# Kernel optimization log

Measured on AMD Instinct MI355X. Metric: run time of the kernel, lower is better.

## Reference

```python
import jax, jax.numpy as jnp
import numpy as np
import math


def proxy_delta_linear(x, W, gain):
    # x: [B,T,Din], W: [Dout,Din], gain: [1,1,Dout]
    D = x.shape[-1]
    xa = jnp.tanh(x)
    wa = jnp.tanh(W)
    x_sq = jnp.sum(xa * xa, axis=-1, keepdims=True)          # [B,T,1]
    w_sq = jnp.sum(wa * wa, axis=-1)                          # [Dout]
    dot = jnp.einsum('btd,od->bto', xa, wa)                   # [B,T,Dout]
    l2_sq = jnp.clip(x_sq + w_sq - 2.0 * dot, 0.0)
    out = 1.0 - l2_sq / D
    return (out - 0.5) * gain


def setup_inputs() -> dict:
    key = jax.random.key(0)
    ks = jax.random.split(key, 6)
    B, T, C = 2, 2048, 1024
    return {
        'x':  jax.random.normal(ks[0], (B, T, C), dtype=jnp.float32),
        'Wq': jax.random.normal(ks[1], (C, C), dtype=jnp.float32) * 0.02,
        'gq': jnp.full((1, 1, C), 2.0, dtype=jnp.float32),
        'Wk': jax.random.normal(ks[2], (C, C), dtype=jnp.float32) * 0.02,
        'gk': jnp.full((1, 1, C), 2.0, dtype=jnp.float32),
        'Wv': jax.random.normal(ks[3], (C, C), dtype=jnp.float32) * 0.02,
        'gv': jnp.full((1, 1, C), 2.0, dtype=jnp.float32),
        'Wo': jax.random.normal(ks[4], (C, C), dtype=jnp.float32) * 0.02,
    }


def reference(x, Wq, gq, Wk, gk, Wv, gv, Wo):
    B, T, C = x.shape
    H = 16
    D = C // H
    scale = math.sqrt(D)
    q = jnp.tanh(proxy_delta_linear(x, Wq, gq)).reshape(B, T, H, D).transpose(0, 2, 1, 3)
    k = jnp.tanh(proxy_delta_linear(x, Wk, gk)).reshape(B, T, H, D).transpose(0, 2, 1, 3)
    v = proxy_delta_linear(x, Wv, gv).reshape(B, T, H, D).transpose(0, 2, 1, 3)
    q_sq = jnp.sum(q * q, axis=-1, keepdims=True)             # [B,H,T,1]
    k_sq = jnp.sum(k * k, axis=-1)[:, :, None, :]             # [B,H,1,T]
    dot = jnp.einsum('bhtd,bhsd->bhts', q, k)                 # [B,H,T,T]
    dist_sq = jnp.clip(q_sq + k_sq - 2.0 * dot, 0.0)
    logits = -dist_sq / (scale * 10.0)
    attn = jax.nn.softmax(logits, axis=-1)
    out = jnp.einsum('bhts,bhsd->bhtd', attn, v)
    out = out.transpose(0, 2, 1, 3).reshape(B, T, C)
    return jnp.einsum('btc,oc->bto', out, Wo)
```

## Files before the change

kernel.cpp:

```cpp
#include <hip/hip_runtime.h>
#include <hip/hip_bf16.h>
#include <math.h>

typedef unsigned short u16;
typedef unsigned int u32;
typedef __attribute__((ext_vector_type(8))) short short8;
typedef __attribute__((ext_vector_type(8))) unsigned short ushort8;
typedef __attribute__((ext_vector_type(4))) float floatx4;
typedef __attribute__((ext_vector_type(16))) float floatx16;
typedef __attribute__((ext_vector_type(4))) u32 uint4v;

#define CDIM   1024
#define TSEQ   2048
#define NHEAD  16
#define HDIM   64

#define C2_CONST  (-0.01803368801111874f)
#define M2C2_CONST (0.03606737602223748f)

static __device__ __forceinline__ u16 f2bf(float f) {
    u32 u = __float_as_uint(f);
    u += 0x7fffu + ((u >> 16) & 1u);
    return (u16)(u >> 16);
}

static __device__ __forceinline__ u32 cvtpk(float a, float b) {
    u32 r;
    asm("v_cvt_pk_bf16_f32 %0, %1, %2" : "=v"(r) : "v"(a), "v"(b));
    return r;
}

static __device__ __forceinline__ float ftanh(float x) {
    float e = exp2f(x * 2.88539008f);
    float r = __builtin_amdgcn_rcpf(e + 1.0f);
    return fmaf(-2.0f, r, 1.0f);
}

static __device__ __forceinline__ void gll16(const void* g, void* l) {
    __builtin_amdgcn_global_load_lds(
        (const __attribute__((address_space(1))) unsigned int*)g,
        (__attribute__((address_space(3))) unsigned int*)l, 16, 0, 0);
}

__global__ __launch_bounds__(256) void prep(const float* __restrict__ x,
                                            const float* __restrict__ Wq, const float* __restrict__ Wk,
                                            const float* __restrict__ Wv, const float* __restrict__ Wo,
                                            u16* __restrict__ xa,
                                            u16* __restrict__ waq, u16* __restrict__ wak,
                                            u16* __restrict__ wav, u16* __restrict__ wob,
                                            float* __restrict__ xsq,
                                            float* __restrict__ sqq, float* __restrict__ sqk,
                                            float* __restrict__ sqv) {
    __shared__ float red[4];
    int bid = blockIdx.x, tid = threadIdx.x;
    const float* src; u16* dst; float* sq; int row; bool do_tanh = true;
    if (bid < 4096) {
        row = bid; src = x; dst = xa; sq = xsq;
    } else {
        int mat = (bid - 4096) >> 10; row = (bid - 4096) & 1023;
        src = (mat == 0) ? Wq : (mat == 1) ? Wk : (mat == 2) ? Wv : Wo;
        dst = (mat == 0) ? waq : (mat == 1) ? wak : (mat == 2) ? wav : wob;
        sq  = (mat == 0) ? sqq : (mat == 1) ? sqk : (mat == 2) ? sqv : nullptr;
        do_tanh = (mat < 3);
    }
    float4 v = reinterpret_cast<const float4*>(src + (size_t)row * CDIM)[tid];
    if (do_tanh) {
        float a0 = ftanh(v.x), a1 = ftanh(v.y), a2 = ftanh(v.z), a3 = ftanh(v.w);
        *reinterpret_cast<ushort4*>(dst + (size_t)row * CDIM + tid * 4) =
            make_ushort4(f2bf(a0), f2bf(a1), f2bf(a2), f2bf(a3));
        float s = a0*a0 + a1*a1 + a2*a2 + a3*a3;
        #pragma unroll
        for (int m = 1; m < 64; m <<= 1) s += __shfl_xor(s, m, 64);
        if ((tid & 63) == 0) red[tid >> 6] = s;
        __syncthreads();
        if (tid == 0 && sq) sq[row] = red[0] + red[1] + red[2] + red[3];
    } else {
        *reinterpret_cast<ushort4*>(dst + (size_t)row * CDIM + tid * 4) =
            make_ushort4(f2bf(v.x), f2bf(v.y), f2bf(v.z), f2bf(v.w));
    }
}

__global__ __launch_bounds__(256) void gemm_qkv(const u16* __restrict__ xa,
                                                const u16* __restrict__ waq, const u16* __restrict__ wak, const u16* __restrict__ wav,
                                                u16* __restrict__ qF, u16* __restrict__ kF, u16* __restrict__ vF,
                                                const float* __restrict__ xsq,
                                                const float* __restrict__ sqq, const float* __restrict__ sqk, const float* __restrict__ sqv,
                                                const float* __restrict__ gq, const float* __restrict__ gk, const float* __restrict__ gv,
                                                float* __restrict__ ksC2T) {
    __shared__ __align__(16) u16 As[128 * 64];
    __shared__ __align__(16) u16 Bs[128 * 64];
    int z = blockIdx.z;
    const u16* Bm     = (z == 0) ? waq : (z == 1) ? wak : wav;
    const float* wsq  = (z == 0) ? sqq : (z == 1) ? sqk : sqv;
    const float* gain = (z == 0) ? gq : (z == 1) ? gk : gv;

    int tid = threadIdx.x;
    int m0 = blockIdx.y * 128, n0 = blockIdx.x * 128;
    int w = tid >> 6, l = tid & 63, wm = w >> 1, wn = w & 1, g = l >> 4, c = l & 15;
    int r8 = l >> 3, sl7 = l & 7;
    int cmask = (c & 7) ^ (c >> 3);

    floatx4 acc[4][4] = {};

    for (int kt = 0; kt < 16; ++kt) {
        __syncthreads();
        #pragma unroll
        for (int i = 0; i < 4; i++) {
            int ch = w * 4 + i;
            int row = ch * 8 + r8;
            int sl = sl7 ^ r8 ^ (ch & 1);
            gll16(xa + (size_t)(m0 + row) * CDIM + kt * 64 + sl * 8, &As[ch * 512 + l * 8]);
            gll16(Bm + (size_t)(n0 + row) * CDIM + kt * 64 + sl * 8, &Bs[ch * 512 + l * 8]);
        }
        __syncthreads();
        short8 af[2][4], bf[2][4];
        #pragma unroll
        for (int kk = 0; kk < 2; kk++) {
            #pragma unroll
            for (int mi = 0; mi < 4; mi++)
                af[kk][mi] = *reinterpret_cast<const short8*>(
                    &As[(wm * 64 + mi * 16 + c) * 64 + (((kk * 4 + g) ^ cmask) << 3)]);
            #pragma unroll
            for (int ni = 0; ni < 4; ni++)
                bf[kk][ni] = *reinterpret_cast<const short8*>(
                    &Bs[(wn * 64 + ni * 16 + c) * 64 + (((kk * 4 + g) ^ cmask) << 3)]);
        }
        #pragma unroll
        for (int kk = 0; kk < 2; kk++)
            #pragma unroll
            for (int mi = 0; mi < 4; mi++)
                #pragma unroll
                for (int ni = 0; ni < 4; ni++)
                    acc[mi][ni] = __builtin_amdgcn_mfma_f32_16x16x32_bf16(af[kk][mi], bf[kk][ni], acc[mi][ni], 0, 0, 0);
    }

    if (z < 2) {
        u16* outF = (z == 0) ? qF : kF;
        float part[4][4] = {};
        #pragma unroll
        for (int mi = 0; mi < 4; mi++) {
            int rowb = m0 + wm * 64 + mi * 16 + g * 4;
            int bb = rowb >> 11, tt = rowb & 2047;
            int tile = tt >> 5, l31 = tt & 31;
            #pragma unroll
            for (int ni = 0; ni < 4; ni++) {
                int col = n0 + wn * 64 + ni * 16 + c;
                int hh = col >> 6, d = col & 63;
                int kst = d >> 4, hi8 = (d >> 3) & 1, j = d & 7;
                size_t base = ((((size_t)(bb * NHEAD + hh) * 64 + tile) * 4 + kst) * 2 + hi8) * 256 + j;
                float wsqc = wsq[col], gn = gain[col];
                #pragma unroll
                for (int r = 0; r < 4; r++) {
                    float l2 = fmaxf(xsq[rowb + r] + wsqc - 2.f * acc[mi][ni][r], 0.f);
                    float th = ftanh((0.5f - l2 * (1.f / 1024.f)) * gn);
                    outF[base + (size_t)(l31 + r) * 8] = f2bf(th);
                    part[mi][r] += th * th;
                }
            }
        }
        if (z == 1) {
            int hh = blockIdx.x * 2 + wn;
            #pragma unroll
            for (int mi = 0; mi < 4; mi++)
                #pragma unroll
                for (int r = 0; r < 4; r++) {
                    float s = part[mi][r];
                    s += __shfl_xor(s, 1, 64); s += __shfl_xor(s, 2, 64);
                    s += __shfl_xor(s, 4, 64); s += __shfl_xor(s, 8, 64);
                    if (c == 0) {
                        int row = m0 + wm * 64 + mi * 16 + g * 4 + r;
                        int bb = row >> 11, t = row & 2047;
                        ksC2T[(size_t)(bb * NHEAD + hh) * TSEQ + t] = s * C2_CONST;
                    }
                }
        }
    } else {
        #pragma unroll
        for (int mi = 0; mi < 4; mi++) {
            int rowb = m0 + wm * 64 + mi * 16 + g * 4;
            int bb = rowb >> 11, s = rowb & 2047;
            int tile = s >> 5, e = (s >> 4) & 1, hi8 = (s >> 3) & 1, j0 = s & 7;
            #pragma unroll
            for (int ni = 0; ni < 4; ni++) {
                int col = n0 + wn * 64 + ni * 16 + c;
                int hh = col >> 6, d = col & 63;
                int dt = d >> 5, l31 = d & 31;
                float wsqc = wsq[col], gn = gain[col];
                float vals[4];
                #pragma unroll
                for (int r = 0; r < 4; r++) {
                    float l2 = fmaxf(xsq[rowb + r] + wsqc - 2.f * acc[mi][ni][r], 0.f);
                    vals[r] = (0.5f - l2 * (1.f / 1024.f)) * gn;
                }
                size_t idx = (((((size_t)(bb * NHEAD + hh) * 2 + dt) * 64 + tile) * 2 + e) * 2 + hi8) * 256
                             + (size_t)l31 * 8 + j0;
                *reinterpret_cast<ushort4*>(&vF[idx]) =
                    make_ushort4(f2bf(vals[0]), f2bf(vals[1]), f2bf(vals[2]), f2bf(vals[3]));
            }
        }
    }
}

__global__ __launch_bounds__(256) void gemm_out(const u16* __restrict__ A, const u16* __restrict__ Bm,
                                                float* __restrict__ outF) {
    __shared__ __align__(16) u16 As[128 * 64];
    __shared__ __align__(16) u16 Bs[128 * 64];
    int tid = threadIdx.x;
    int m0 = blockIdx.y * 128, n0 = blockIdx.x * 128;
    int w = tid >> 6, l = tid & 63, wm = w >> 1, wn = w & 1, g = l >> 4, c = l & 15;
    int r8 = l >> 3, sl7 = l & 7;
    int cmask = (c & 7) ^ (c >> 3);

    floatx4 acc[4][4] = {};

    for (int kt = 0; kt < 16; ++kt) {
        __syncthreads();
        #pragma unroll
        for (int i = 0; i < 4; i++) {
            int ch = w * 4 + i;
            int row = ch * 8 + r8;
            int sl = sl7 ^ r8 ^ (ch & 1);
            gll16(A + (size_t)(m0 + row) * CDIM + kt * 64 + sl * 8, &As[ch * 512 + l * 8]);
            gll16(Bm + (size_t)(n0 + row) * CDIM + kt * 64 + sl * 8, &Bs[ch * 512 + l * 8]);
        }
        __syncthreads();
        short8 af[2][4], bf[2][4];
        #pragma unroll
        for (int kk = 0; kk < 2; kk++) {
            #pragma unroll
            for (int mi = 0; mi < 4; mi++)
                af[kk][mi] = *reinterpret_cast<const short8*>(
                    &As[(wm * 64 + mi * 16 + c) * 64 + (((kk * 4 + g) ^ cmask) << 3)]);
            #pragma unroll
            for (int ni = 0; ni < 4; ni++)
                bf[kk][ni] = *reinterpret_cast<const short8*>(
                    &Bs[(wn * 64 + ni * 16 + c) * 64 + (((kk * 4 + g) ^ cmask) << 3)]);
        }
        #pragma unroll
        for (int kk = 0; kk < 2; kk++)
            #pragma unroll
            for (int mi = 0; mi < 4; mi++)
                #pragma unroll
                for (int ni = 0; ni < 4; ni++)
                    acc[mi][ni] = __builtin_amdgcn_mfma_f32_16x16x32_bf16(af[kk][mi], bf[kk][ni], acc[mi][ni], 0, 0, 0);
    }

    #pragma unroll
    for (int mi = 0; mi < 4; mi++) {
        int rowb = m0 + wm * 64 + mi * 16 + g * 4;
        #pragma unroll
        for (int ni = 0; ni < 4; ni++) {
            int col = n0 + wn * 64 + ni * 16 + c;
            #pragma unroll
            for (int r = 0; r < 4; r++)
                outF[(size_t)(rowb + r) * CDIM + col] = acc[mi][ni][r];
        }
    }
}

__global__ __launch_bounds__(256, 4) void attn9(const u16* __restrict__ qF, const u16* __restrict__ kF,
                                                const u16* __restrict__ vF,
                                                const float* __restrict__ ksC2T, u16* __restrict__ ao) {
    int bid = blockIdx.x;
    int hb = bid & 31;
    int ttile = bid >> 5;
    int tid = threadIdx.x, sc = tid >> 6, l = tid & 63;
    int hi = l >> 5, t32 = l & 31;

    __shared__ float redO[2][64][33];
    __shared__ float Ls[32];

    const u16* qbase = qF + ((size_t)hb * 64 + ttile) * 2048;
    short8 qf[4];
    #pragma unroll
    for (int ks = 0; ks < 4; ks++)
        qf[ks] = *reinterpret_cast<const short8*>(qbase + ks * 512 + (size_t)l * 8);

    const u16* kbase = kF + (size_t)hb * (64 * 2048);
    const u16* vbase = vF + (size_t)hb * (2 * 64 * 1024);
    const float* ksb = ksC2T + (size_t)hb * TSEQ;

    floatx16 oacc[2] = {};
    float lrun = 0.f;

    int st0 = sc * 16;
    for (int st = st0; st < st0 + 16; ++st) {
        const short8* kp = reinterpret_cast<const short8*>(kbase + (size_t)st * 2048) + l;
        short8 kf0 = kp[0], kf1 = kp[64], kf2 = kp[128], kf3 = kp[192];
        const short8* vp = reinterpret_cast<const short8*>(vbase + (size_t)st * 1024) + l;
        short8 vf00 = vp[0], vf01 = vp[64];
        short8 vf10 = vp[8192], vf11 = vp[8256];

        floatx16 sxx = {};
        sxx = __builtin_amdgcn_mfma_f32_32x32x16_bf16(kf0, qf[0], sxx, 0, 0, 0);
        sxx = __builtin_amdgcn_mfma_f32_32x32x16_bf16(kf1, qf[1], sxx, 0, 0, 0);
        sxx = __builtin_amdgcn_mfma_f32_32x32x16_bf16(kf2, qf[2], sxx, 0, 0, 0);
        sxx = __builtin_amdgcn_mfma_f32_32x32x16_bf16(kf3, qf[3], sxx, 0, 0, 0);

        u32 pk[8];
        #pragma unroll
        for (int qq = 0; qq < 4; qq++) {
            float4 kc = *reinterpret_cast<const float4*>(&ksb[st * 32 + qq * 8 + hi * 4]);
            float p0 = exp2f(fmaf(sxx[qq * 4 + 0], M2C2_CONST, kc.x));
            float p1 = exp2f(fmaf(sxx[qq * 4 + 1], M2C2_CONST, kc.y));
            float p2 = exp2f(fmaf(sxx[qq * 4 + 2], M2C2_CONST, kc.z));
            float p3 = exp2f(fmaf(sxx[qq * 4 + 3], M2C2_CONST, kc.w));
            lrun += (p0 + p1) + (p2 + p3);
            pk[qq * 2]     = cvtpk(p0, p1);
            pk[qq * 2 + 1] = cvtpk(p2, p3);
        }

        u32 ex[4];
        #pragma unroll
        for (int m = 0; m < 4; m++) {
            const int p0a[4] = {0, 1, 4, 5};
            u32 send = hi ? pk[p0a[m]] : pk[p0a[m] + 2];
            ex[m] = (u32)__shfl_xor((int)send, 32, 64);
        }

        #pragma unroll
        for (int e = 0; e < 2; e++) {
            uint4v au;
            au.x = hi ? ex[2 * e]     : pk[4 * e];
            au.y = hi ? ex[2 * e + 1] : pk[4 * e + 1];
            au.z = hi ? pk[4 * e + 2] : ex[2 * e];
            au.w = hi ? pk[4 * e + 3] : ex[2 * e + 1];
            short8 af = __builtin_bit_cast(short8, au);
            oacc[0] = __builtin_amdgcn_mfma_f32_32x32x16_bf16(af, e ? vf01 : vf00, oacc[0], 0, 0, 0);
            oacc[1] = __builtin_amdgcn_mfma_f32_32x32x16_bf16(af, e ? vf11 : vf10, oacc[1], 0, 0, 0);
        }
    }

    if (sc == 1 || sc == 3) {
        int sid = sc >> 1;
        #pragma unroll
        for (int dt = 0; dt < 2; dt++)
            #pragma unroll
            for (int r = 0; r < 16; r++)
                redO[sid][l][dt * 16 + r] = oacc[dt][r];
        redO[sid][l][32] = lrun;
    }
    __syncthreads();
    if (sc == 0 || sc == 2) {
        int sid = sc >> 1;
        #pragma unroll
        for (int dt = 0; dt < 2; dt++)
            #pragma unroll
            for (int r = 0; r < 16; r++)
                oacc[dt][r] += redO[sid][l][dt * 16 + r];
        lrun += redO[sid][l][32];
    }
    __syncthreads();
    if (sc == 2) {
        #pragma unroll
        for (int dt = 0; dt < 2; dt++)
            #pragma unroll
            for (int r = 0; r < 16; r++)
                redO[0][l][dt * 16 + r] = oacc[dt][r];
        redO[0][l][32] = lrun;
    }
    __syncthreads();
    if (sc == 0) {
        #pragma unroll
        for (int dt = 0; dt < 2; dt++)
            #pragma unroll
            for (int r = 0; r < 16; r++)
                oacc[dt][r] += redO[0][l][dt * 16 + r];
        lrun += redO[0][l][32];

        float ltot = lrun + __shfl_xor(lrun, 32, 64);
        if (l < 32) Ls[l] = ltot;
        int b = hb >> 4, h = hb & 15;
        int twb = ttile * 32;
        float4 lv[4];
        #pragma unroll
        for (int qq = 0; qq < 4; qq++)
            lv[qq] = *reinterpret_cast<const float4*>(&Ls[qq * 8 + hi * 4]);
        #pragma unroll
        for (int dt = 0; dt < 2; dt++)
            #pragma unroll
            for (int r = 0; r < 16; ++r) {
                int trow = (r & 3) + 8 * (r >> 2) + 4 * hi;
                float lval = (r & 3) == 0 ? lv[r >> 2].x : (r & 3) == 1 ? lv[r >> 2].y
                           : (r & 3) == 2 ? lv[r >> 2].z : lv[r >> 2].w;
                ao[(size_t)(b * TSEQ + twb + trow) * CDIM + h * HDIM + dt * 32 + t32] =
                    f2bf(oacc[dt][r] * __builtin_amdgcn_rcpf(lval));
            }
    }
}

extern "C" void kernel_launch(void* const* d_in, const int* in_sizes, int n_in,
                              void* d_out, int out_size, void* d_ws, size_t ws_size,
                              hipStream_t stream) {
    const float* x  = (const float*)d_in[0];
    const float* Wq = (const float*)d_in[1];
    const float* gq = (const float*)d_in[2];
    const float* Wk = (const float*)d_in[3];
    const float* gk = (const float*)d_in[4];
    const float* Wv = (const float*)d_in[5];
    const float* gv = (const float*)d_in[6];
    const float* Wo = (const float*)d_in[7];
    float* out = (float*)d_out;

    char* p = (char*)d_ws;
    u16* xa  = (u16*)p;  p += (size_t)8 << 20;
    u16* qF  = (u16*)p;  p += (size_t)8 << 20;
    u16* kF  = (u16*)p;  p += (size_t)8 << 20;
    u16* vF  = (u16*)p;  p += (size_t)8 << 20;
    u16* ao  = (u16*)p;  p += (size_t)8 << 20;
    u16* waq = (u16*)p;  p += (size_t)2 << 20;
    u16* wak = (u16*)p;  p += (size_t)2 << 20;
    u16* wav = (u16*)p;  p += (size_t)2 << 20;
    u16* wob = (u16*)p;  p += (size_t)2 << 20;
    float* xsq   = (float*)p; p += 4096 * 4;
    float* sqq   = (float*)p; p += 1024 * 4;
    float* sqk   = (float*)p; p += 1024 * 4;
    float* sqv   = (float*)p; p += 1024 * 4;
    float* ksC2T = (float*)p; p += 4096 * 16 * 4;
    (void)ws_size; (void)in_sizes; (void)n_in; (void)out_size;

    prep<<<8192, 256, 0, stream>>>(x, Wq, Wk, Wv, Wo, xa, waq, wak, wav, wob,
                                   xsq, sqq, sqk, sqv);

    dim3 gqkv(8, 32, 3);
    gemm_qkv<<<gqkv, 256, 0, stream>>>(xa, waq, wak, wav, qF, kF, vF, xsq,
                                       sqq, sqk, sqv, gq, gk, gv, ksC2T);

    attn9<<<2048, 256, 0, stream>>>(qF, kF, vF, ksC2T, ao);

    dim3 gg(8, 32);
    gemm_out<<<gg, 256, 0, stream>>>(ao, wob, out);
}
```

Before: 141.0 us.

## Use permlane32_swap and setprio in attention; compute key norms in separate kernel

The attention inner loop now exchanges P fragments between wave halves with permlane32_swap instead of four shfl_xor calls, and raises wave priority around the MFMA sections with s_setprio. It also uses packed float2 FMA and accumulation, and unrolls the loop by two. The key squared-norm calculation moves out of the QKV GEMM epilogue into a new small kernel that reads the bf16 K values back. This trims the GEMM epilogue but adds an extra launch and read pass, and the norms are now computed from rounded bf16 values, which changes numerics slightly.

```diff
diff --git a/kernel.cpp b/kernel.cpp
--- a/kernel.cpp
+++ b/kernel.cpp
@@ -9,6 +9,8 @@
 typedef __attribute__((ext_vector_type(4))) float floatx4;
 typedef __attribute__((ext_vector_type(16))) float floatx16;
 typedef __attribute__((ext_vector_type(4))) u32 uint4v;
+typedef __attribute__((ext_vector_type(2))) float float2v;
+typedef __attribute__((ext_vector_type(2))) int int2v;
 
 #define CDIM   1024
 #define TSEQ   2048
@@ -22,6 +24,9 @@
     u32 u = __float_as_uint(f);
     u += 0x7fffu + ((u >> 16) & 1u);
     return (u16)(u >> 16);
+}
+static __device__ __forceinline__ float bf2f(u16 h) {
+    return __uint_as_float(((u32)h) << 16);
 }
 
 static __device__ __forceinline__ u32 cvtpk(float a, float b) {
@@ -85,8 +90,7 @@
                                                 u16* __restrict__ qF, u16* __restrict__ kF, u16* __restrict__ vF,
                                                 const float* __restrict__ xsq,
                                                 const float* __restrict__ sqq, const float* __restrict__ sqk, const float* __restrict__ sqv,
-                                                const float* __restrict__ gq, const float* __restrict__ gk, const float* __restrict__ gv,
-                                                float* __restrict__ ksC2T) {
+                                                const float* __restrict__ gq, const float* __restrict__ gk, const float* __restrict__ gv) {
     __shared__ __align__(16) u16 As[128 * 64];
     __shared__ __align__(16) u16 Bs[128 * 64];
     int z = blockIdx.z;
@@ -136,7 +140,6 @@
 
     if (z < 2) {
         u16* outF = (z == 0) ? qF : kF;
-        float part[4][4] = {};
         #pragma unroll
         for (int mi = 0; mi < 4; mi++) {
             int rowb = m0 + wm * 64 + mi * 16 + g * 4;
@@ -154,25 +157,8 @@
                     float l2 = fmaxf(xsq[rowb + r] + wsqc - 2.f * acc[mi][ni][r], 0.f);
                     float th = ftanh((0.5f - l2 * (1.f / 1024.f)) * gn);
                     outF[base + (size_t)(l31 + r) * 8] = f2bf(th);
-                    part[mi][r] += th * th;
                 }
             }
-        }
-        if (z == 1) {
-            int hh = blockIdx.x * 2 + wn;
-            #pragma unroll
-            for (int mi = 0; mi < 4; mi++)
-                #pragma unroll
-                for (int r = 0; r < 4; r++) {
-                    float s = part[mi][r];
-                    s += __shfl_xor(s, 1, 64); s += __shfl_xor(s, 2, 64);
-                    s += __shfl_xor(s, 4, 64); s += __shfl_xor(s, 8, 64);
-                    if (c == 0) {
-                        int row = m0 + wm * 64 + mi * 16 + g * 4 + r;
-                        int bb = row >> 11, t = row & 2047;
-                        ksC2T[(size_t)(bb * NHEAD + hh) * TSEQ + t] = s * C2_CONST;
-                    }
-                }
         }
     } else {
         #pragma unroll
@@ -201,6 +187,23 @@
     }
 }
 
+__global__ __launch_bounds__(256) void knorm(const u16* __restrict__ kF,
+                                             float* __restrict__ ksC2T) {
+    int hb = blockIdx.x >> 3, seg = blockIdx.x & 7;
+    int tile = seg * 8 + (threadIdx.x >> 5), t32 = threadIdx.x & 31;
+    const u16* base = kF + ((size_t)hb * 64 + tile) * 2048 + t32 * 8;
+    float s = 0.f;
+    #pragma unroll
+    for (int kst = 0; kst < 4; kst++)
+        #pragma unroll
+        for (int hi8 = 0; hi8 < 2; hi8++) {
+            ushort8 v = *reinterpret_cast<const ushort8*>(base + (kst * 2 + hi8) * 256);
+            #pragma unroll
+            for (int j = 0; j < 8; j++) { float f = bf2f(v[j]); s += f * f; }
+        }
+    ksC2T[(size_t)hb * TSEQ + tile * 32 + t32] = s * C2_CONST;
+}
+
 __global__ __launch_bounds__(256) void gemm_out(const u16* __restrict__ A, const u16* __restrict__ Bm,
                                                 float* __restrict__ outF) {
     __shared__ __align__(16) u16 As[128 * 64];
@@ -258,9 +261,9 @@
     }
 }
 
-__global__ __launch_bounds__(256, 4) void attn9(const u16* __restrict__ qF, const u16* __restrict__ kF,
-                                                const u16* __restrict__ vF,
-                                                const float* __restrict__ ksC2T, u16* __restrict__ ao) {
+__global__ __launch_bounds__(256, 4) void attn10(const u16* __restrict__ qF, const u16* __restrict__ kF,
+                                                 const u16* __restrict__ vF,
+                                                 const float* __restrict__ ksC2T, u16* __restrict__ ao) {
     int bid = blockIdx.x;
     int hb = bid & 31;
     int ttile = bid >> 5;
@@ -281,9 +284,11 @@
     const float* ksb = ksC2T + (size_t)hb * TSEQ;
 
     floatx16 oacc[2] = {};
-    float lrun = 0.f;
+    float2v l2a = {0.f, 0.f};
+    const float2v m2v = {M2C2_CONST, M2C2_CONST};
 
     int st0 = sc * 16;
+    #pragma unroll 2
     for (int st = st0; st < st0 + 16; ++st) {
         const short8* kp = reinterpret_cast<const short8*>(kbase + (size_t)st * 2048) + l;
         short8 kf0 = kp[0], kf1 = kp[64], kf2 = kp[128], kf3 = kp[192];
@@ -291,45 +296,47 @@
         short8 vf00 = vp[0], vf01 = vp[64];
         short8 vf10 = vp[8192], vf11 = vp[8256];
 
+        __builtin_amdgcn_s_setprio(1);
         floatx16 sxx = {};
         sxx = __builtin_amdgcn_mfma_f32_32x32x16_bf16(kf0, qf[0], sxx, 0, 0, 0);
         sxx = __builtin_amdgcn_mfma_f32_32x32x16_bf16(kf1, qf[1], sxx, 0, 0, 0);
         sxx = __builtin_amdgcn_mfma_f32_32x32x16_bf16(kf2, qf[2], sxx, 0, 0, 0);
         sxx = __builtin_amdgcn_mfma_f32_32x32x16_bf16(kf3, qf[3], sxx, 0, 0, 0);
+        __builtin_amdgcn_s_setprio(0);
 
         u32 pk[8];
         #pragma unroll
         for (int qq = 0; qq < 4; qq++) {
             float4 kc = *reinterpret_cast<const float4*>(&ksb[st * 32 + qq * 8 + hi * 4]);
-            float p0 = exp2f(fmaf(sxx[qq * 4 + 0], M2C2_CONST, kc.x));
-            float p1 = exp2f(fmaf(sxx[qq * 4 + 1], M2C2_CONST, kc.y));
-            float p2 = exp2f(fmaf(sxx[qq * 4 + 2], M2C2_CONST, kc.z));
-            float p3 = exp2f(fmaf(sxx[qq * 4 + 3], M2C2_CONST, kc.w));
-            lrun += (p0 + p1) + (p2 + p3);
+            float2v s01 = {sxx[qq * 4 + 0], sxx[qq * 4 + 1]};
+            float2v s23 = {sxx[qq * 4 + 2], sxx[qq * 4 + 3]};
+            float2v a01 = s01 * m2v + (float2v){kc.x, kc.y};
+            float2v a23 = s23 * m2v + (float2v){kc.z, kc.w};
+            float p0 = exp2f(a01.x), p1 = exp2f(a01.y);
+            float p2 = exp2f(a23.x), p3 = exp2f(a23.y);
+            l2a += (float2v){p0, p1};
+            l2a += (float2v){p2, p3};
             pk[qq * 2]     = cvtpk(p0, p1);
             pk[qq * 2 + 1] = cvtpk(p2, p3);
         }
 
-        u32 ex[4];
-        #pragma unroll
-        for (int m = 0; m < 4; m++) {
-            const int p0a[4] = {0, 1, 4, 5};
-            u32 send = hi ? pk[p0a[m]] : pk[p0a[m] + 2];
-            ex[m] = (u32)__shfl_xor((int)send, 32, 64);
-        }
-
+        __builtin_amdgcn_s_setprio(1);
         #pragma unroll
         for (int e = 0; e < 2; e++) {
+            int2v r02 = __builtin_amdgcn_permlane32_swap((int)pk[4 * e + 2], (int)pk[4 * e + 0], false, false);
+            int2v r13 = __builtin_amdgcn_permlane32_swap((int)pk[4 * e + 3], (int)pk[4 * e + 1], false, false);
             uint4v au;
-            au.x = hi ? ex[2 * e]     : pk[4 * e];
-            au.y = hi ? ex[2 * e + 1] : pk[4 * e + 1];
-            au.z = hi ? pk[4 * e + 2] : ex[2 * e];
-            au.w = hi ? pk[4 * e + 3] : ex[2 * e + 1];
+            au.x = (u32)r02.y;
+            au.y = (u32)r13.y;
+            au.z = (u32)r02.x;
+            au.w = (u32)r13.x;
             short8 af = __builtin_bit_cast(short8, au);
             oacc[0] = __builtin_amdgcn_mfma_f32_32x32x16_bf16(af, e ? vf01 : vf00, oacc[0], 0, 0, 0);
             oacc[1] = __builtin_amdgcn_mfma_f32_32x32x16_bf16(af, e ? vf11 : vf10, oacc[1], 0, 0, 0);
         }
-    }
+        __builtin_amdgcn_s_setprio(0);
+    }
+    float lrun = l2a.x + l2a.y;
 
     if (sc == 1 || sc == 3) {
         int sid = sc >> 1;
@@ -424,9 +431,11 @@
 
     dim3 gqkv(8, 32, 3);
     gemm_qkv<<<gqkv, 256, 0, stream>>>(xa, waq, wak, wav, qF, kF, vF, xsq,
-                                       sqq, sqk, sqv, gq, gk, gv, ksC2T);
-
-    attn9<<<2048, 256, 0, stream>>>(qF, kF, vF, ksC2T, ao);
+                                       sqq, sqk, sqv, gq, gk, gv);
+
+    knorm<<<256, 256, 0, stream>>>(kF, ksC2T);
+
+    attn10<<<2048, 256, 0, stream>>>(qF, kF, vF, ksC2T, ao);
 
     dim3 gg(8, 32);
     gemm_out<<<gg, 256, 0, stream>>>(ao, wob, out);
```

New measurement: 143.0 us. No clear change (+1.4%).
